# Optimization experiments

Hardware: AMD Instinct MI355X
Metric: run time of the kernel (lower is better)

The kernel has to match this reference:

```python
import jax, jax.numpy as jnp
import numpy as np

B, S, H = 2, 2048, 2048
DK = DV = 128
HK, HV = 16, 32
G = HV // HK          # num_v_groups = 2
K = 4                 # conv kernel size
EPS = 1e-6
FQKVZ = 2 * HK * DK + 2 * HV * DV   # 12288
FBA = 2 * HV                        # 64
C = 2 * HK * DK + HV * DV           # conv channels = 8192


def setup_inputs() -> dict:
    key = jax.random.key(0)
    ks = jax.random.split(key, 10)
    f32 = jnp.float32
    return {
        "x": jax.random.normal(ks[0], (B, S, H), f32),
        "w_qkvz": jax.random.normal(ks[1], (H, FQKVZ), f32) * 0.02,
        "w_ba": jax.random.normal(ks[2], (H, FBA), f32) * 0.02,
        "conv_w": jax.random.normal(ks[3], (C, K), f32) * 0.1,
        "conv_b": jax.random.normal(ks[4], (C,), f32) * 0.02,
        "a_log": jax.random.normal(ks[5], (HV,), f32) * 0.5,
        "dt_bias": jax.random.normal(ks[6], (HV,), f32) * 0.5,
        "norm_w": jnp.ones((DV,), f32),
        "w_o": jax.random.normal(ks[7], (HV * DV, H), f32) * 0.02,
    }


def _l2norm(t):
    return t * jax.lax.rsqrt(jnp.sum(t * t, axis=-1, keepdims=True) + EPS)


def reference(x, w_qkvz, w_ba, conv_w, conv_b, a_log, dt_bias, norm_w, w_o):
    # fused input projections
    qkvz = x @ w_qkvz                                   # [B,S,FQKVZ]
    ba = x @ w_ba                                       # [B,S,FBA]

    # split_fused_inputs: per k-head layout [q(DK), k(DK), v(G*DV), z(G*DV)]
    qkvz = qkvz.reshape(B, S, HK, 2 * DK + 2 * G * DV)
    q = qkvz[..., :DK]                                  # [B,S,HK,DK]
    k = qkvz[..., DK:2 * DK]
    v = qkvz[..., 2 * DK:2 * DK + G * DV].reshape(B, S, HV, DV)
    z = qkvz[..., 2 * DK + G * DV:].reshape(B, S, HV, DV)
    ba = ba.reshape(B, S, HK, 2 * G)
    b = ba[..., :G].reshape(B, S, HV)
    a = ba[..., G:].reshape(B, S, HV)

    # causal depthwise conv1d + silu over concat(q,k,v) channels
    mixed = jnp.concatenate(
        [q.reshape(B, S, HK * DK), k.reshape(B, S, HK * DK), v.reshape(B, S, HV * DV)],
        axis=-1).transpose(0, 2, 1)                     # [B,C,S]
    mixed = jnp.pad(mixed, ((0, 0), (0, 0), (K - 1, 0)))
    mixed = jax.lax.conv_general_dilated(
        mixed, conv_w[:, None, :], (1,), 'VALID',
        dimension_numbers=('NCH', 'OIH', 'NCH'), feature_group_count=C)
    mixed = jax.nn.silu(mixed + conv_b[None, :, None]).transpose(0, 2, 1)  # [B,S,C]

    kd = HK * DK
    q = mixed[..., :kd].reshape(B, S, HK, DK)
    k = mixed[..., kd:2 * kd].reshape(B, S, HK, DK)
    v = mixed[..., 2 * kd:].reshape(B, S, HV, DV)

    # gating params
    g = -jnp.exp(a_log) * jax.nn.softplus(a + dt_bias)  # [B,S,HV]
    beta = jax.nn.sigmoid(b)                            # [B,S,HV]

    # GQA expand + qk l2-norm (kernel applies l2norm inside)
    q = jnp.repeat(q, G, axis=2)                        # [B,S,HV,DK]
    k = jnp.repeat(k, G, axis=2)
    q = _l2norm(q) * (DK ** -0.5)
    k = _l2norm(k)

    # gated delta-rule recurrence: S_t = exp(g_t) S_{t-1} + k_t (beta_t (v_t - k_t^T S))
    def step(Sm, inp):
        q_t, k_t, v_t, g_t, b_t = inp                   # [B,HV,*]
        Sm = Sm * jnp.exp(g_t)[..., None, None]
        kS = jnp.einsum('bhk,bhkv->bhv', k_t, Sm)
        dv = b_t[..., None] * (v_t - kS)
        Sm = Sm + k_t[..., None] * dv[:, :, None, :]
        o_t = jnp.einsum('bhk,bhkv->bhv', q_t, Sm)
        return Sm, o_t

    S0 = jnp.zeros((B, HV, DK, DV), q.dtype)
    seq = (jnp.moveaxis(q, 1, 0), jnp.moveaxis(k, 1, 0), jnp.moveaxis(v, 1, 0),
           jnp.moveaxis(g, 1, 0), jnp.moveaxis(beta, 1, 0))
    _, o = jax.lax.scan(step, S0, seq)                  # o: [S,B,HV,DV]
    o = jnp.moveaxis(o, 0, 1)                           # [B,S,HV,DV]

    # gated RMSNorm (Mamba-style: gate before norm)
    y = o * jax.nn.silu(z)
    var = jnp.mean(y * y, axis=-1, keepdims=True)
    y = y * jax.lax.rsqrt(var + EPS) * norm_w

    return y.reshape(B, S, HV * DV) @ w_o               # [B,S,H]
```

## Files before the change

### kernel.cpp

```cpp
#include <hip/hip_runtime.h>

typedef _Float16 f16;
typedef _Float16 f16x2 __attribute__((ext_vector_type(2)));
typedef _Float16 f16x4 __attribute__((ext_vector_type(4)));
typedef _Float16 f16x8 __attribute__((ext_vector_type(8)));
typedef float f32x4 __attribute__((ext_vector_type(4)));

#define QSCALE 0.08838834764831845f

#define RAW_BARRIER() do { \
    asm volatile("s_waitcnt lgkmcnt(0)" ::: "memory"); \
    __builtin_amdgcn_s_barrier(); \
    __builtin_amdgcn_sched_barrier(0); \
} while (0)

__global__ __launch_bounds__(256) void cvt16_kernel(const float* __restrict__ in,
                                                    f16* __restrict__ out, int n4) {
    int i = blockIdx.x * 256 + threadIdx.x;
    if (i >= n4) return;
    f32x4 v = ((const f32x4*)in)[i];
    f16x4 h;
    h[0] = (f16)v[0]; h[1] = (f16)v[1]; h[2] = (f16)v[2]; h[3] = (f16)v[3];
    ((f16x4*)out)[i] = h;
}

__global__ __launch_bounds__(256) void transpose16_kernel(const float* __restrict__ in,
                                                          f16* __restrict__ out, int R, int C) {
    __shared__ f16 tile[64][66];
    int c0 = blockIdx.x * 64, r0 = blockIdx.y * 64;
    int tid = threadIdx.x;
#pragma unroll
    for (int i = 0; i < 16; ++i) {
        int idx = i * 256 + tid;
        int r = idx >> 6, c = idx & 63;
        tile[r][c] = (f16)in[(long)(r0 + r) * C + (c0 + c)];
    }
    __syncthreads();
#pragma unroll
    for (int i = 0; i < 16; ++i) {
        int idx = i * 256 + tid;
        int orow = idx >> 6, oc = idx & 63;
        out[(long)(c0 + orow) * R + (r0 + oc)] = tile[oc][orow];
    }
}

template <int NJ, int F16OUT>
__global__ __launch_bounds__(512, 1) void gemm256_kernel(const f16* __restrict__ A,
                                                         const f16* __restrict__ Bt,
                                                         void* __restrict__ Cout,
                                                         int M, int N, int Kd) {
    constexpr int BN = 64 * NJ;
    constexpr int BNW = 16 * NJ;
    __shared__ f16 sA[2][256 * 64];
    __shared__ f16 sB[2][BN * 64];
    const int tid = threadIdx.x;
    const int lane = tid & 63, wv = tid >> 6;
    const int wm = wv >> 2, wn = wv & 3;
    const int m0 = blockIdx.y * 256, n0 = blockIdx.x * BN;
    const int lrow = lane & 15, lk = lane >> 4;
    const int nK = Kd >> 6;

    f32x4 acc[8][NJ] = {};
    f32x4 ra[4], rb[NJ];

    auto issue = [&](int k0) {
#pragma unroll
        for (int j = 0; j < 4; ++j) {
            int P = (tid + j * 512) * 16;
            int row = P >> 7;
            int koff = (P & 127) >> 1;
            ra[j] = *(const f32x4*)(A + (long)(m0 + row) * Kd + k0 + koff);
        }
#pragma unroll
        for (int j = 0; j < NJ; ++j) {
            int P = (tid + j * 512) * 16;
            int row = P >> 7;
            int koff = (P & 127) >> 1;
            rb[j] = *(const f32x4*)(Bt + (long)(n0 + row) * Kd + k0 + koff);
        }
    };
    auto commit = [&](int buf) {
#pragma unroll
        for (int j = 0; j < 4; ++j) {
            int P = (tid + j * 512) * 16;
            int row = P >> 7;
            int sw = P ^ ((row & 7) << 4);
            *(f32x4*)((char*)&sA[buf][0] + sw) = ra[j];
        }
#pragma unroll
        for (int j = 0; j < NJ; ++j) {
            int P = (tid + j * 512) * 16;
            int row = P >> 7;
            int sw = P ^ ((row & 7) << 4);
            *(f32x4*)((char*)&sB[buf][0] + sw) = rb[j];
        }
    };

    issue(0);
    commit(0);
    if (nK > 1) issue(64);
    RAW_BARRIER();

    int cur = 0;
    for (int t = 0; t < nK; ++t) {
        if (t + 1 < nK) commit(cur ^ 1);
        if (t + 2 < nK) issue((t + 2) * 64);
        const char* bA = (const char*)&sA[cur][0];
        const char* bB = (const char*)&sB[cur][0];
        __builtin_amdgcn_s_setprio(1);
#pragma unroll
        for (int kk = 0; kk < 2; ++kk) {
            f16x8 bf[NJ];
#pragma unroll
            for (int j = 0; j < NJ; ++j) {
                int brow = wn * BNW + j * 16 + lrow;
                int bbyte = brow * 128 + kk * 64 + lk * 16;
                bf[j] = *(const f16x8*)(bB + (bbyte ^ ((brow & 7) << 4)));
            }
#pragma unroll
            for (int i = 0; i < 8; ++i) {
                int arow = wm * 128 + i * 16 + lrow;
                int abyte = arow * 128 + kk * 64 + lk * 16;
                f16x8 af = *(const f16x8*)(bA + (abyte ^ ((arow & 7) << 4)));
#pragma unroll
                for (int j = 0; j < NJ; ++j)
                    acc[i][j] = __builtin_amdgcn_mfma_f32_16x16x32_f16(af, bf[j], acc[i][j], 0, 0, 0);
            }
        }
        __builtin_amdgcn_s_setprio(0);
        RAW_BARRIER();
        cur ^= 1;
    }

#pragma unroll
    for (int i = 0; i < 8; ++i) {
        int gm_base = m0 + wm * 128 + i * 16 + lk * 4;
#pragma unroll
        for (int j = 0; j < NJ; ++j) {
            int gn = n0 + wn * BNW + j * 16 + lrow;
#pragma unroll
            for (int r = 0; r < 4; ++r) {
                long idx = (long)(gm_base + r) * N + gn;
                if (F16OUT) ((f16*)Cout)[idx] = (f16)acc[i][j][r];
                else        ((float*)Cout)[idx] = acc[i][j][r];
            }
        }
    }
}

__global__ __launch_bounds__(256) void ba_gemm_kernel(const float* __restrict__ x,
                                                      const float* __restrict__ w,
                                                      const float* __restrict__ a_log,
                                                      const float* __restrict__ dt_bias,
                                                      float* __restrict__ gout,
                                                      float* __restrict__ bt) {
    __shared__ float xs[16][256];
    int tid = threadIdx.x;
    int t0 = blockIdx.x * 16;
    int o = tid & 63, tg = tid >> 6;
    float acc[4] = {0.f, 0.f, 0.f, 0.f};
    for (int kc = 0; kc < 2048; kc += 256) {
        __syncthreads();
#pragma unroll
        for (int i = 0; i < 16; ++i) {
            int idx = i * 256 + tid;
            int tok = idx >> 8, k = idx & 255;
            xs[tok][k] = x[(long)(t0 + tok) * 2048 + kc + k];
        }
        __syncthreads();
        for (int k = 0; k < 256; ++k) {
            float wv = w[(long)(kc + k) * 64 + o];
#pragma unroll
            for (int j = 0; j < 4; ++j) acc[j] += xs[tg * 4 + j][k] * wv;
        }
    }
    int hv = ((o >> 2) << 1) | (o & 1);
    bool isB = (o & 2) == 0;
    float al = expf(a_log[hv]);
    float db = dt_bias[hv];
#pragma unroll
    for (int j = 0; j < 4; ++j) {
        int tok = t0 + tg * 4 + j;
        int b = tok >> 11, s = tok & 2047;
        long oidx = ((long)b * 32 + hv) * 2048 + s;
        if (isB) {
            bt[oidx] = 1.f / (1.f + expf(-acc[j]));
        } else {
            float xx = acc[j] + db;
            float sp = (xx > 20.f) ? xx : log1pf(expf(xx));
            gout[oidx] = -al * sp;
        }
    }
}

__global__ __launch_bounds__(256) void conv_kernel(const f16* __restrict__ qkvz,
                                                   const float* __restrict__ cw,
                                                   const float* __restrict__ cb,
                                                   f16* __restrict__ qh,
                                                   f16* __restrict__ kh,
                                                   f16* __restrict__ vh) {
    __shared__ float Lin[35 * 128];
    __shared__ float Lout[32 * 128];
    __shared__ float Lsc[32];
    int g = blockIdx.x;
    int s0 = blockIdx.y * 32;
    int b = blockIdx.z;
    int tid = threadIdx.x;
    int colbase, chbase;
    f16* outp;
    bool donorm;
    float nmul;
    if (g < 16) {
        colbase = g * 768; chbase = g * 128;
        outp = qh + (((long)b * 16 + g) * 2048 + s0) * 128;
        donorm = true; nmul = QSCALE;
    } else if (g < 32) {
        int hk = g - 16;
        colbase = hk * 768 + 128; chbase = 2048 + hk * 128;
        outp = kh + (((long)b * 16 + hk) * 2048 + s0) * 128;
        donorm = true; nmul = 1.f;
    } else {
        int hv = g - 32;
        colbase = (hv >> 1) * 768 + 256 + (hv & 1) * 128; chbase = 4096 + hv * 128;
        outp = vh + (((long)b * 32 + hv) * 2048 + s0) * 128;
        donorm = false; nmul = 1.f;
    }
    for (int ci = tid; ci < 35 * 16; ci += 256) {
        int sr = ci >> 4, cc = (ci & 15) * 8;
        int s = s0 + sr - 3;
        f32x4 lo = {}, hi = {};
        if (s >= 0) {
            f16x8 v = *(const f16x8*)(qkvz + ((long)b * 2048 + s) * 12288 + colbase + cc);
#pragma unroll
            for (int e = 0; e < 4; ++e) { lo[e] = (float)v[e]; hi[e] = (float)v[4 + e]; }
        }
        *(f32x4*)&Lin[sr * 128 + cc] = lo;
        *(f32x4*)&Lin[sr * 128 + cc + 4] = hi;
    }
    __syncthreads();
    int c = tid & 127, sg = tid >> 7;
    float w0 = cw[(chbase + c) * 4 + 0];
    float w1 = cw[(chbase + c) * 4 + 1];
    float w2 = cw[(chbase + c) * 4 + 2];
    float w3 = cw[(chbase + c) * 4 + 3];
    float bias = cb[chbase + c];
#pragma unroll
    for (int j = 0; j < 16; ++j) {
        int sl = sg * 16 + j;
        float v = w0 * Lin[sl * 128 + c] + w1 * Lin[(sl + 1) * 128 + c] +
                  w2 * Lin[(sl + 2) * 128 + c] + w3 * Lin[(sl + 3) * 128 + c] + bias;
        v = v / (1.f + expf(-v));
        Lout[sl * 128 + c] = v;
    }
    __syncthreads();
    if (donorm) {
        int token = tid >> 3, part = tid & 7;
        float ss = 0.f;
#pragma unroll
        for (int i = 0; i < 16; ++i) {
            float v = Lout[token * 128 + part * 16 + i];
            ss += v * v;
        }
        ss += __shfl_xor(ss, 1); ss += __shfl_xor(ss, 2); ss += __shfl_xor(ss, 4);
        if (part == 0) Lsc[token] = rsqrtf(ss + 1e-6f) * nmul;
        __syncthreads();
#pragma unroll
        for (int j = 0; j < 16; ++j) {
            int sl = sg * 16 + j;
            outp[(long)sl * 128 + c] = (f16)(Lout[sl * 128 + c] * Lsc[sl]);
        }
    } else {
#pragma unroll
        for (int j = 0; j < 16; ++j) {
            int sl = sg * 16 + j;
            outp[(long)sl * 128 + c] = (f16)Lout[sl * 128 + c];
        }
    }
}

__global__ __launch_bounds__(256) void kT_kernel(const f16* __restrict__ kh,
                                                 f16* __restrict__ khT) {
    __shared__ f16 t[64][136];
    int bh = blockIdx.x >> 5;
    int s0 = (blockIdx.x & 31) * 64;
    int tid = threadIdx.x;
#pragma unroll
    for (int it = 0; it < 4; ++it) {
        int P = (tid + it * 256) * 8;
        int r = P >> 7, col = P & 127;
        *(f16x8*)&t[r][col] = *(const f16x8*)(kh + ((long)bh * 2048 + s0 + r) * 128 + col);
    }
    __syncthreads();
#pragma unroll
    for (int it = 0; it < 4; ++it) {
        int Q = (tid + it * 256) * 8;
        int dk = Q >> 6, sc = Q & 63;
        f16x8 v;
#pragma unroll
        for (int e = 0; e < 8; ++e) v[e] = t[sc + e][dk];
        *(f16x8*)(khT + ((long)bh * 128 + dk) * 2048 + s0 + sc) = v;
    }
}

__global__ __launch_bounds__(64) void chunk_pre_kernel(const f16* __restrict__ qh,
                                                       const f16* __restrict__ kh,
                                                       const f16* __restrict__ vh,
                                                       const float* __restrict__ gb,
                                                       const float* __restrict__ bt,
                                                       f16* __restrict__ Wg,
                                                       f16* __restrict__ T2ng,
                                                       f16* __restrict__ d0g,
                                                       float* __restrict__ pvg) {
    __shared__ f16 VTl[128 * 32];
    __shared__ float KKl[32 * 32];
    __shared__ float RL[32 * 32];
    __shared__ float Tf[32 * 33];
    __shared__ f16 Tl[32 * 64];
    __shared__ float cuml[32], bl[32], pl[32];

    int bid = blockIdx.x;
    int chunk = bid & 63;
    int hv = (bid >> 6) & 31;
    int b = bid >> 11;
    int bh = b * 16 + (hv >> 1);
    int l = threadIdx.x;
    int h = l >> 4, c = l & 15;
    long chid = bid;

    const f16* kbase = kh + ((long)bh * 2048 + chunk * 32) * 128;
    const f16* qbase = qh + ((long)bh * 2048 + chunk * 32) * 128;
    const f16* vbase = vh + (((long)b * 32 + hv) * 2048 + chunk * 32) * 128;
    const float* gp = gb + ((long)b * 32 + hv) * 2048 + chunk * 32;
    const float* bp = bt + ((long)b * 32 + hv) * 2048 + chunk * 32;

    f16x8 fk[2][4], fq[2][4];
#pragma unroll
    for (int ti = 0; ti < 2; ++ti)
#pragma unroll
        for (int kk = 0; kk < 4; ++kk) {
            fk[ti][kk] = *(const f16x8*)(kbase + (c + 16 * ti) * 128 + kk * 32 + h * 8);
            fq[ti][kk] = *(const f16x8*)(qbase + (c + 16 * ti) * 128 + kk * 32 + h * 8);
        }

    float gv = (l < 32) ? gp[l] : 0.f;
#pragma unroll
    for (int d = 1; d < 32; d <<= 1) {
        float t2 = __shfl_up(gv, d);
        if (l >= d) gv += t2;
    }
    if (l < 32) { cuml[l] = gv; bl[l] = bp[l]; pl[l] = expf(gv); }
    __syncthreads();

#pragma unroll
    for (int it = 0; it < 8; ++it) {
        int idx = (l + it * 64) * 8;
        int row = idx >> 7, col = idx & 127;
        f16x8 v = *(const f16x8*)(vbase + (long)row * 128 + col);
        float be = bl[row];
#pragma unroll
        for (int e = 0; e < 8; ++e) {
            int dv = col + e;
            int byte = (dv * 64 + row * 2) ^ ((dv & 3) << 4);
            *(f16*)((char*)VTl + byte) = (f16)((float)v[e] * be);
        }
    }
#pragma unroll
    for (int it = 0; it < 16; ++it) {
        int e = l * 16 + it;
        int i = e >> 5, j = e & 31;
        RL[e] = (j <= i) ? expf(cuml[i] - cuml[j]) : 0.f;
    }
    __syncthreads();

    {
        f32x4 acc[2][2] = {};
#pragma unroll
        for (int kk = 0; kk < 4; ++kk) {
            acc[0][0] = __builtin_amdgcn_mfma_f32_16x16x32_f16(fk[0][kk], fk[0][kk], acc[0][0], 0, 0, 0);
            acc[0][1] = __builtin_amdgcn_mfma_f32_16x16x32_f16(fk[0][kk], fk[1][kk], acc[0][1], 0, 0, 0);
            acc[1][0] = __builtin_amdgcn_mfma_f32_16x16x32_f16(fk[1][kk], fk[0][kk], acc[1][0], 0, 0, 0);
            acc[1][1] = __builtin_amdgcn_mfma_f32_16x16x32_f16(fk[1][kk], fk[1][kk], acc[1][1], 0, 0, 0);
        }
#pragma unroll
        for (int ti = 0; ti < 2; ++ti)
#pragma unroll
            for (int tj = 0; tj < 2; ++tj)
#pragma unroll
                for (int r = 0; r < 4; ++r)
                    KKl[(h * 4 + r + 16 * ti) * 32 + c + 16 * tj] = acc[ti][tj][r];
    }
    {
        f32x4 acc[2][2] = {};
#pragma unroll
        for (int kk = 0; kk < 4; ++kk) {
            acc[0][0] = __builtin_amdgcn_mfma_f32_16x16x32_f16(fq[0][kk], fk[0][kk], acc[0][0], 0, 0, 0);
            acc[0][1] = __builtin_amdgcn_mfma_f32_16x16x32_f16(fq[0][kk], fk[1][kk], acc[0][1], 0, 0, 0);
            acc[1][0] = __builtin_amdgcn_mfma_f32_16x16x32_f16(fq[1][kk], fk[0][kk], acc[1][0], 0, 0, 0);
            acc[1][1] = __builtin_amdgcn_mfma_f32_16x16x32_f16(fq[1][kk], fk[1][kk], acc[1][1], 0, 0, 0);
        }
        __syncthreads();
#pragma unroll
        for (int ti = 0; ti < 2; ++ti)
#pragma unroll
            for (int tj = 0; tj < 2; ++tj)
#pragma unroll
                for (int r = 0; r < 4; ++r) {
                    int i = h * 4 + r + 16 * ti, j = c + 16 * tj;
                    Wg[chid * 1024 + i * 32 + j] = (f16)(acc[ti][tj][r] * RL[i * 32 + j]);
                }
    }

    if (l < 32) {
        int j = l;
        for (int i = 0; i < 32; ++i) {
            float s = (i == j) ? 1.f : 0.f;
            float bi = bl[i];
            for (int ll = j; ll < i; ++ll)
                s -= bi * KKl[i * 32 + ll] * RL[i * 32 + ll] * Tf[ll * 33 + j];
            Tf[i * 33 + j] = s;
        }
        float bpj = bl[j] * pl[j];
        for (int i = 0; i < 32; ++i) {
            float tv = (i >= j) ? Tf[i * 33 + j] : 0.f;
            int byte = (i * 128 + j * 2) ^ ((i & 3) << 4);
            *(f16*)((char*)Tl + byte) = (f16)tv;
            T2ng[chid * 1024 + i * 32 + j] = (f16)(-tv * bpj);
        }
        pvg[chid * 64 + j] = pl[j];
        pvg[chid * 64 + 32 + j] = expf(cuml[31] - cuml[j]);
    }
    __syncthreads();

    {
        f16x8 fT[2];
#pragma unroll
        for (int ti = 0; ti < 2; ++ti) {
            int row = c + 16 * ti;
            fT[ti] = *(const f16x8*)((const char*)Tl + ((row * 128 + h * 16) ^ ((row & 3) << 4)));
        }
#pragma unroll
        for (int nj = 0; nj < 8; ++nj) {
            int dv = c + 16 * nj;
            f16x8 fv = *(const f16x8*)((const char*)VTl + ((dv * 64 + h * 16) ^ ((dv & 3) << 4)));
            f32x4 a0 = {}, a1 = {};
            a0 = __builtin_amdgcn_mfma_f32_16x16x32_f16(fT[0], fv, a0, 0, 0, 0);
            a1 = __builtin_amdgcn_mfma_f32_16x16x32_f16(fT[1], fv, a1, 0, 0, 0);
            f16x4 s0, s1;
#pragma unroll
            for (int r = 0; r < 4; ++r) { s0[r] = (f16)a0[r]; s1[r] = (f16)a1[r]; }
            *(f16x4*)(d0g + chid * 4096 + (long)dv * 32 + 4 * h) = s0;
            *(f16x4*)(d0g + chid * 4096 + (long)dv * 32 + 16 + 4 * h) = s1;
        }
    }
}

__global__ __launch_bounds__(64) void scan_kernel(const f16* __restrict__ qh,
                                                  const f16* __restrict__ kh,
                                                  const f16* __restrict__ khT,
                                                  const f16* __restrict__ Wg,
                                                  const f16* __restrict__ T2ng,
                                                  const f16* __restrict__ d0g,
                                                  const float* __restrict__ pvg,
                                                  f16* __restrict__ ob) {
    __shared__ f16 Sl[2][16 * 128];
    __shared__ f16 AKl[16 * 32];
    __shared__ f16 Dl[16 * 32];

    int pbid = blockIdx.x;
    int bid = (pbid & 7) * 64 + (pbid >> 3);
    int vs = bid & 7;
    int hv = (bid >> 3) & 31;
    int b = bid >> 8;
    int bh32 = b * 32 + hv;
    int bh = b * 16 + (hv >> 1);
    int l = threadIdx.x, h = l >> 4, c = l & 15;

    const f16* kb = kh + (long)bh * 2048 * 128;
    const f16* qb = qh + (long)bh * 2048 * 128;
    const f16* ktb = khT + (long)bh * 128 * 2048;

    f16x8 z = {};
#pragma unroll
    for (int it = 0; it < 4; ++it) *(f16x8*)((char*)Sl[0] + (l + it * 64) * 16) = z;
    __syncthreads();

    int cur = 0;
    for (int ch = 0; ch < 64; ++ch) {
        long chid = (long)bh32 * 64 + ch;
        f16x8 fk[2][4], fq[2][4], fkt[8], fT[2], fW[2];
#pragma unroll
        for (int ti = 0; ti < 2; ++ti) {
            long row = ch * 32 + c + 16 * ti;
#pragma unroll
            for (int kk = 0; kk < 4; ++kk) {
                fk[ti][kk] = *(const f16x8*)(kb + row * 128 + kk * 32 + h * 8);
                fq[ti][kk] = *(const f16x8*)(qb + row * 128 + kk * 32 + h * 8);
            }
            fT[ti] = *(const f16x8*)(T2ng + chid * 1024 + (c + 16 * ti) * 32 + h * 8);
            fW[ti] = *(const f16x8*)(Wg + chid * 1024 + (c + 16 * ti) * 32 + h * 8);
        }
#pragma unroll
        for (int ti = 0; ti < 8; ++ti)
            fkt[ti] = *(const f16x8*)(ktb + (long)(c + 16 * ti) * 2048 + ch * 32 + h * 8);
        f16x4 fd0[2];
#pragma unroll
        for (int ti = 0; ti < 2; ++ti)
            fd0[ti] = *(const f16x4*)(d0g + chid * 4096 +
                                      (long)(vs * 16 + c) * 32 + 16 * ti + 4 * h);
        f32x4 pva = *(const f32x4*)(pvg + chid * 64 + 4 * h);
        f32x4 pvb = *(const f32x4*)(pvg + chid * 64 + 16 + 4 * h);
        float pc = pvg[chid * 64 + 31];
        f32x4 kwa = *(const f32x4*)(pvg + chid * 64 + 32 + h * 8);
        f32x4 kwb = *(const f32x4*)(pvg + chid * 64 + 36 + h * 8);

        const int dv = c;
        f16x8 fS[4];
#pragma unroll
        for (int kk = 0; kk < 4; ++kk)
            fS[kk] = *(const f16x8*)((char*)Sl[cur] +
                                     (dv * 256 + ((kk * 64 + h * 16) ^ ((dv & 7) << 4))));
        f32x4 AK[2] = {}, AQ[2] = {};
#pragma unroll
        for (int ti = 0; ti < 2; ++ti)
#pragma unroll
            for (int kk = 0; kk < 4; ++kk) {
                AK[ti] = __builtin_amdgcn_mfma_f32_16x16x32_f16(fk[ti][kk], fS[kk], AK[ti], 0, 0, 0);
                AQ[ti] = __builtin_amdgcn_mfma_f32_16x16x32_f16(fq[ti][kk], fS[kk], AQ[ti], 0, 0, 0);
            }
#pragma unroll
        for (int ti = 0; ti < 2; ++ti) {
            f16x4 t;
#pragma unroll
            for (int r = 0; r < 4; ++r) t[r] = (f16)AK[ti][r];
            *(f16x4*)((char*)AKl + ((dv * 64 + 32 * ti + 8 * h) ^ ((dv & 3) << 4))) = t;
        }
        f32x4 Dv[2];
#pragma unroll
        for (int ti = 0; ti < 2; ++ti)
#pragma unroll
            for (int r = 0; r < 4; ++r) Dv[ti][r] = (float)fd0[ti][r];
        {
            f16x8 fak = *(const f16x8*)((char*)AKl + ((dv * 64 + h * 16) ^ ((dv & 3) << 4)));
#pragma unroll
            for (int ti = 0; ti < 2; ++ti)
                Dv[ti] = __builtin_amdgcn_mfma_f32_16x16x32_f16(fT[ti], fak, Dv[ti], 0, 0, 0);
        }
#pragma unroll
        for (int ti = 0; ti < 2; ++ti) {
            f16x4 t;
#pragma unroll
            for (int r = 0; r < 4; ++r) t[r] = (f16)Dv[ti][r];
            *(f16x4*)((char*)Dl + ((dv * 64 + 32 * ti + 8 * h) ^ ((dv & 3) << 4))) = t;
        }
        f16x8 fdl = *(const f16x8*)((char*)Dl + ((dv * 64 + h * 16) ^ ((dv & 3) << 4)));
        f32x4 Ov[2];
#pragma unroll
        for (int ti = 0; ti < 2; ++ti)
#pragma unroll
            for (int r = 0; r < 4; ++r)
                Ov[ti][r] = AQ[ti][r] * (ti ? pvb[r] : pva[r]);
#pragma unroll
        for (int ti = 0; ti < 2; ++ti)
            Ov[ti] = __builtin_amdgcn_mfma_f32_16x16x32_f16(fW[ti], fdl, Ov[ti], 0, 0, 0);
#pragma unroll
        for (int ti = 0; ti < 2; ++ti)
#pragma unroll
            for (int r = 0; r < 4; ++r) {
                long tok = (long)b * 2048 + ch * 32 + 16 * ti + 4 * h + r;
                ob[tok * 4096 + hv * 128 + vs * 16 + c] = (f16)Ov[ti][r];
            }
#pragma unroll
        for (int ti = 0; ti < 8; ++ti) {
            f16x8 fa;
#pragma unroll
            for (int e = 0; e < 8; ++e)
                fa[e] = (f16)((float)fkt[ti][e] * (e < 4 ? kwa[e] : kwb[e - 4]));
            int sbyte = (dv * 256 + (32 * ti + 8 * h)) ^ ((dv & 7) << 4);
            f16x4 sold = *(const f16x4*)((char*)Sl[cur] + sbyte);
            f32x4 acc;
#pragma unroll
            for (int r = 0; r < 4; ++r) acc[r] = pc * (float)sold[r];
            acc = __builtin_amdgcn_mfma_f32_16x16x32_f16(fa, fdl, acc, 0, 0, 0);
            f16x4 snew;
#pragma unroll
            for (int r = 0; r < 4; ++r) snew[r] = (f16)acc[r];
            *(f16x4*)((char*)Sl[cur ^ 1] + sbyte) = snew;
        }
        cur ^= 1;
        __syncthreads();
    }
}

__global__ __launch_bounds__(256) void gate_kernel(const f16* __restrict__ o,
                                                   const f16* __restrict__ qkvz,
                                                   const float* __restrict__ norm_w,
                                                   f16* __restrict__ y) {
    int token = blockIdx.x;
    int tid = threadIdx.x;
    int hv = tid >> 3, part = tid & 7;
    int dv0 = part * 16;
    const f16* orow = o + ((long)token * 32 + hv) * 128 + dv0;
    long zcol = (long)(hv >> 1) * 768 + 512 + (hv & 1) * 128 + dv0;
    const f16* zrow = qkvz + (long)token * 12288 + zcol;
    f16x8 ov0 = *(const f16x8*)orow, ov1 = *(const f16x8*)(orow + 8);
    f16x8 zv0 = *(const f16x8*)zrow, zv1 = *(const f16x8*)(zrow + 8);
    float yv[16];
    float ss = 0.f;
#pragma unroll
    for (int i = 0; i < 16; ++i) {
        float ovf = (float)(i < 8 ? ov0[i] : ov1[i - 8]);
        float zvf = (float)(i < 8 ? zv0[i] : zv1[i - 8]);
        float gt = zvf / (1.f + expf(-zvf));
        float v = ovf * gt;
        yv[i] = v;
        ss += v * v;
    }
    ss += __shfl_xor(ss, 1); ss += __shfl_xor(ss, 2); ss += __shfl_xor(ss, 4);
    float scale = rsqrtf(ss * (1.f / 128.f) + 1e-6f);
    f16* yrow = y + (long)token * 4096 + hv * 128 + dv0;
    f16x8 y0, y1;
#pragma unroll
    for (int i = 0; i < 8; ++i) {
        y0[i] = (f16)(yv[i] * scale * norm_w[dv0 + i]);
        y1[i] = (f16)(yv[8 + i] * scale * norm_w[dv0 + 8 + i]);
    }
    *(f16x8*)yrow = y0;
    *(f16x8*)(yrow + 8) = y1;
}

extern "C" void kernel_launch(void* const* d_in, const int* in_sizes, int n_in,
                              void* d_out, int out_size, void* d_ws, size_t ws_size,
                              hipStream_t stream) {
    const float* x       = (const float*)d_in[0];
    const float* w_qkvz  = (const float*)d_in[1];
    const float* w_ba    = (const float*)d_in[2];
    const float* conv_w  = (const float*)d_in[3];
    const float* conv_b  = (const float*)d_in[4];
    const float* a_log   = (const float*)d_in[5];
    const float* dt_bias = (const float*)d_in[6];
    const float* norm_w  = (const float*)d_in[7];
    const float* w_o     = (const float*)d_in[8];
    float* out = (float*)d_out;

    char* ws = (char*)d_ws;
    const size_t MB = 1024 * 1024;
    f16*   qkvz16 = (f16*)ws;
    f16*   x16    = (f16*)(ws + 96 * MB);
    f16*   WT     = (f16*)(ws + 112 * MB);
    f16*   d0g    = (f16*)(ws + 96 * MB);
    f16*   Wg     = (f16*)(ws + 128 * MB);
    f16*   T2ng   = (f16*)(ws + 136 * MB);
    f16*   khT    = (f16*)(ws + 144 * MB);
    f16*   WTo    = (f16*)(ws + 160 * MB);
    f16*   qh     = (f16*)(ws + 176 * MB);
    f16*   kh     = (f16*)(ws + 192 * MB);
    f16*   vh     = (f16*)(ws + 208 * MB);
    f16*   ob     = (f16*)(ws + 208 * MB);
    f16*   y16    = (f16*)(ws + 176 * MB);
    float* gbuf   = (float*)(ws + 240 * MB);
    float* btb    = (float*)(ws + 240 * MB + 512 * 1024);
    float* pvg    = (float*)(ws + 241 * MB);

    cvt16_kernel<<<8192, 256, 0, stream>>>(x, x16, 4096 * 2048 / 4);
    transpose16_kernel<<<dim3(12288 / 64, 2048 / 64), 256, 0, stream>>>(w_qkvz, WT, 2048, 12288);
    transpose16_kernel<<<dim3(2048 / 64, 4096 / 64), 256, 0, stream>>>(w_o, WTo, 4096, 2048);

    gemm256_kernel<4, 1><<<dim3(12288 / 256, 4096 / 256), 512, 0, stream>>>(x16, WT, qkvz16, 4096, 12288, 2048);
    ba_gemm_kernel<<<256, 256, 0, stream>>>(x, w_ba, a_log, dt_bias, gbuf, btb);

    conv_kernel<<<dim3(64, 64, 2), 256, 0, stream>>>(qkvz16, conv_w, conv_b, qh, kh, vh);
    kT_kernel<<<1024, 256, 0, stream>>>(kh, khT);
    chunk_pre_kernel<<<4096, 64, 0, stream>>>(qh, kh, vh, gbuf, btb, Wg, T2ng, d0g, pvg);
    scan_kernel<<<512, 64, 0, stream>>>(qh, kh, khT, Wg, T2ng, d0g, pvg, ob);

    gate_kernel<<<4096, 256, 0, stream>>>(ob, qkvz16, norm_w, y16);

    gemm256_kernel<2, 0><<<dim3(2048 / 128, 4096 / 256), 512, 0, stream>>>(y16, WTo, out, 4096, 2048, 4096);
}
```

Measured before the change: 820.9 us.

## Fuse k transpose into conv and software-pipeline scan chunk loads

The conv kernel now also writes the transposed, normalized k (khT) straight from shared memory, which removes the separate kT_kernel launch and its extra read/write pass over k. The scan kernel is restructured so the global loads for the next chunk are issued into a second register set while the current chunk computes (double-buffered registers), and it uses raw barriers with launch_bounds(64,1). This should hide global load latency on the serial chunk recurrence. The cost is higher register pressure, and the khT writes in conv are strided 16-byte stores.

```diff
diff --git a/kernel.cpp b/kernel.cpp
--- a/kernel.cpp
+++ b/kernel.cpp
@@ -198,7 +198,8 @@
                                                    const float* __restrict__ cb,
                                                    f16* __restrict__ qh,
                                                    f16* __restrict__ kh,
-                                                   f16* __restrict__ vh) {
+                                                   f16* __restrict__ vh,
+                                                   f16* __restrict__ khT) {
     __shared__ float Lin[35 * 128];
     __shared__ float Lout[32 * 128];
     __shared__ float Lsc[32];
@@ -209,16 +210,18 @@
     int colbase, chbase;
     f16* outp;
     bool donorm;
+    bool isk = false;
+    int hk = 0;
     float nmul;
     if (g < 16) {
         colbase = g * 768; chbase = g * 128;
         outp = qh + (((long)b * 16 + g) * 2048 + s0) * 128;
         donorm = true; nmul = QSCALE;
     } else if (g < 32) {
-        int hk = g - 16;
+        hk = g - 16;
         colbase = hk * 768 + 128; chbase = 2048 + hk * 128;
         outp = kh + (((long)b * 16 + hk) * 2048 + s0) * 128;
-        donorm = true; nmul = 1.f;
+        donorm = true; nmul = 1.f; isk = true;
     } else {
         int hv = g - 32;
         colbase = (hv >> 1) * 768 + 256 + (hv & 1) * 128; chbase = 4096 + hv * 128;
@@ -269,36 +272,24 @@
             int sl = sg * 16 + j;
             outp[(long)sl * 128 + c] = (f16)(Lout[sl * 128 + c] * Lsc[sl]);
         }
+        if (isk) {
+            int dk = tid >> 1, sh = tid & 1;
+            f16x8 v0, v1;
+#pragma unroll
+            for (int i = 0; i < 8; ++i) {
+                v0[i] = (f16)(Lout[(sh * 16 + i) * 128 + dk] * Lsc[sh * 16 + i]);
+                v1[i] = (f16)(Lout[(sh * 16 + 8 + i) * 128 + dk] * Lsc[sh * 16 + 8 + i]);
+            }
+            f16* kt = khT + ((long)(b * 16 + hk) * 128 + dk) * 2048 + s0 + sh * 16;
+            *(f16x8*)kt = v0;
+            *(f16x8*)(kt + 8) = v1;
+        }
     } else {
 #pragma unroll
         for (int j = 0; j < 16; ++j) {
             int sl = sg * 16 + j;
             outp[(long)sl * 128 + c] = (f16)Lout[sl * 128 + c];
         }
-    }
-}
-
-__global__ __launch_bounds__(256) void kT_kernel(const f16* __restrict__ kh,
-                                                 f16* __restrict__ khT) {
-    __shared__ f16 t[64][136];
-    int bh = blockIdx.x >> 5;
-    int s0 = (blockIdx.x & 31) * 64;
-    int tid = threadIdx.x;
-#pragma unroll
-    for (int it = 0; it < 4; ++it) {
-        int P = (tid + it * 256) * 8;
-        int r = P >> 7, col = P & 127;
-        *(f16x8*)&t[r][col] = *(const f16x8*)(kh + ((long)bh * 2048 + s0 + r) * 128 + col);
-    }
-    __syncthreads();
-#pragma unroll
-    for (int it = 0; it < 4; ++it) {
-        int Q = (tid + it * 256) * 8;
-        int dk = Q >> 6, sc = Q & 63;
-        f16x8 v;
-#pragma unroll
-        for (int e = 0; e < 8; ++e) v[e] = t[sc + e][dk];
-        *(f16x8*)(khT + ((long)bh * 128 + dk) * 2048 + s0 + sc) = v;
     }
 }
 
@@ -454,14 +445,21 @@
     }
 }
 
-__global__ __launch_bounds__(64) void scan_kernel(const f16* __restrict__ qh,
-                                                  const f16* __restrict__ kh,
-                                                  const f16* __restrict__ khT,
-                                                  const f16* __restrict__ Wg,
-                                                  const f16* __restrict__ T2ng,
-                                                  const f16* __restrict__ d0g,
-                                                  const float* __restrict__ pvg,
-                                                  f16* __restrict__ ob) {
+struct CR {
+    f16x8 fk[2][4], fq[2][4], fkt[8], fT[2], fW[2];
+    f16x4 fd0[2];
+    f32x4 pva, pvb, kwa, kwb;
+    float pc;
+};
+
+__global__ __launch_bounds__(64, 1) void scan_kernel(const f16* __restrict__ qh,
+                                                     const f16* __restrict__ kh,
+                                                     const f16* __restrict__ khT,
+                                                     const f16* __restrict__ Wg,
+                                                     const f16* __restrict__ T2ng,
+                                                     const f16* __restrict__ d0g,
+                                                     const float* __restrict__ pvg,
+                                                     f16* __restrict__ ob) {
     __shared__ f16 Sl[2][16 * 128];
     __shared__ f16 AKl[16 * 32];
     __shared__ f16 Dl[16 * 32];
@@ -482,37 +480,37 @@
     f16x8 z = {};
 #pragma unroll
     for (int it = 0; it < 4; ++it) *(f16x8*)((char*)Sl[0] + (l + it * 64) * 16) = z;
-    __syncthreads();
 
     int cur = 0;
-    for (int ch = 0; ch < 64; ++ch) {
+
+    auto loadC = [&](CR& R, int ch) {
         long chid = (long)bh32 * 64 + ch;
-        f16x8 fk[2][4], fq[2][4], fkt[8], fT[2], fW[2];
 #pragma unroll
         for (int ti = 0; ti < 2; ++ti) {
-            long row = ch * 32 + c + 16 * ti;
+            long row = (long)ch * 32 + c + 16 * ti;
 #pragma unroll
             for (int kk = 0; kk < 4; ++kk) {
-                fk[ti][kk] = *(const f16x8*)(kb + row * 128 + kk * 32 + h * 8);
-                fq[ti][kk] = *(const f16x8*)(qb + row * 128 + kk * 32 + h * 8);
+                R.fk[ti][kk] = *(const f16x8*)(kb + row * 128 + kk * 32 + h * 8);
+                R.fq[ti][kk] = *(const f16x8*)(qb + row * 128 + kk * 32 + h * 8);
             }
-            fT[ti] = *(const f16x8*)(T2ng + chid * 1024 + (c + 16 * ti) * 32 + h * 8);
-            fW[ti] = *(const f16x8*)(Wg + chid * 1024 + (c + 16 * ti) * 32 + h * 8);
+            R.fT[ti] = *(const f16x8*)(T2ng + chid * 1024 + (c + 16 * ti) * 32 + h * 8);
+            R.fW[ti] = *(const f16x8*)(Wg + chid * 1024 + (c + 16 * ti) * 32 + h * 8);
         }
 #pragma unroll
         for (int ti = 0; ti < 8; ++ti)
-            fkt[ti] = *(const f16x8*)(ktb + (long)(c + 16 * ti) * 2048 + ch * 32 + h * 8);
-        f16x4 fd0[2];
-#pragma unroll
-        for (int ti = 0; ti < 2; ++ti)
-            fd0[ti] = *(const f16x4*)(d0g + chid * 4096 +
-                                      (long)(vs * 16 + c) * 32 + 16 * ti + 4 * h);
-        f32x4 pva = *(const f32x4*)(pvg + chid * 64 + 4 * h);
-        f32x4 pvb = *(const f32x4*)(pvg + chid * 64 + 16 + 4 * h);
-        float pc = pvg[chid * 64 + 31];
-        f32x4 kwa = *(const f32x4*)(pvg + chid * 64 + 32 + h * 8);
-        f32x4 kwb = *(const f32x4*)(pvg + chid * 64 + 36 + h * 8);
-
+            R.fkt[ti] = *(const f16x8*)(ktb + (long)(c + 16 * ti) * 2048 + ch * 32 + h * 8);
+#pragma unroll
+        for (int ti = 0; ti < 2; ++ti)
+            R.fd0[ti] = *(const f16x4*)(d0g + chid * 4096 +
+                                        (long)(vs * 16 + c) * 32 + 16 * ti + 4 * h);
+        R.pva = *(const f32x4*)(pvg + chid * 64 + 4 * h);
+        R.pvb = *(const f32x4*)(pvg + chid * 64 + 16 + 4 * h);
+        R.pc = pvg[chid * 64 + 31];
+        R.kwa = *(const f32x4*)(pvg + chid * 64 + 32 + h * 8);
+        R.kwb = *(const f32x4*)(pvg + chid * 64 + 36 + h * 8);
+    };
+
+    auto computeC = [&](const CR& R, int ch) {
         const int dv = c;
         f16x8 fS[4];
 #pragma unroll
@@ -524,8 +522,8 @@
         for (int ti = 0; ti < 2; ++ti)
 #pragma unroll
             for (int kk = 0; kk < 4; ++kk) {
-                AK[ti] = __builtin_amdgcn_mfma_f32_16x16x32_f16(fk[ti][kk], fS[kk], AK[ti], 0, 0, 0);
-                AQ[ti] = __builtin_amdgcn_mfma_f32_16x16x32_f16(fq[ti][kk], fS[kk], AQ[ti], 0, 0, 0);
+                AK[ti] = __builtin_amdgcn_mfma_f32_16x16x32_f16(R.fk[ti][kk], fS[kk], AK[ti], 0, 0, 0);
+                AQ[ti] = __builtin_amdgcn_mfma_f32_16x16x32_f16(R.fq[ti][kk], fS[kk], AQ[ti], 0, 0, 0);
             }
 #pragma unroll
         for (int ti = 0; ti < 2; ++ti) {
@@ -538,12 +536,12 @@
 #pragma unroll
         for (int ti = 0; ti < 2; ++ti)
 #pragma unroll
-            for (int r = 0; r < 4; ++r) Dv[ti][r] = (float)fd0[ti][r];
+            for (int r = 0; r < 4; ++r) Dv[ti][r] = (float)R.fd0[ti][r];
         {
             f16x8 fak = *(const f16x8*)((char*)AKl + ((dv * 64 + h * 16) ^ ((dv & 3) << 4)));
 #pragma unroll
             for (int ti = 0; ti < 2; ++ti)
-                Dv[ti] = __builtin_amdgcn_mfma_f32_16x16x32_f16(fT[ti], fak, Dv[ti], 0, 0, 0);
+                Dv[ti] = __builtin_amdgcn_mfma_f32_16x16x32_f16(R.fT[ti], fak, Dv[ti], 0, 0, 0);
         }
 #pragma unroll
         for (int ti = 0; ti < 2; ++ti) {
@@ -558,10 +556,10 @@
         for (int ti = 0; ti < 2; ++ti)
 #pragma unroll
             for (int r = 0; r < 4; ++r)
-                Ov[ti][r] = AQ[ti][r] * (ti ? pvb[r] : pva[r]);
-#pragma unroll
-        for (int ti = 0; ti < 2; ++ti)
-            Ov[ti] = __builtin_amdgcn_mfma_f32_16x16x32_f16(fW[ti], fdl, Ov[ti], 0, 0, 0);
+                Ov[ti][r] = AQ[ti][r] * (ti ? R.pvb[r] : R.pva[r]);
+#pragma unroll
+        for (int ti = 0; ti < 2; ++ti)
+            Ov[ti] = __builtin_amdgcn_mfma_f32_16x16x32_f16(R.fW[ti], fdl, Ov[ti], 0, 0, 0);
 #pragma unroll
         for (int ti = 0; ti < 2; ++ti)
 #pragma unroll
@@ -574,12 +572,12 @@
             f16x8 fa;
 #pragma unroll
             for (int e = 0; e < 8; ++e)
-                fa[e] = (f16)((float)fkt[ti][e] * (e < 4 ? kwa[e] : kwb[e - 4]));
+                fa[e] = (f16)((float)R.fkt[ti][e] * (e < 4 ? R.kwa[e] : R.kwb[e - 4]));
             int sbyte = (dv * 256 + (32 * ti + 8 * h)) ^ ((dv & 7) << 4);
             f16x4 sold = *(const f16x4*)((char*)Sl[cur] + sbyte);
             f32x4 acc;
 #pragma unroll
-            for (int r = 0; r < 4; ++r) acc[r] = pc * (float)sold[r];
+            for (int r = 0; r < 4; ++r) acc[r] = R.pc * (float)sold[r];
             acc = __builtin_amdgcn_mfma_f32_16x16x32_f16(fa, fdl, acc, 0, 0, 0);
             f16x4 snew;
 #pragma unroll
@@ -587,7 +585,17 @@
             *(f16x4*)((char*)Sl[cur ^ 1] + sbyte) = snew;
         }
         cur ^= 1;
-        __syncthreads();
+        RAW_BARRIER();
+    };
+
+    CR A, B;
+    loadC(A, 0);
+    RAW_BARRIER();
+    for (int ch = 0; ch < 64; ch += 2) {
+        loadC(B, ch + 1);
+        computeC(A, ch);
+        loadC(A, ch + 2 < 64 ? ch + 2 : 63);
+        computeC(B, ch + 1);
     }
 }
 
@@ -668,8 +676,7 @@
     gemm256_kernel<4, 1><<<dim3(12288 / 256, 4096 / 256), 512, 0, stream>>>(x16, WT, qkvz16, 4096, 12288, 2048);
     ba_gemm_kernel<<<256, 256, 0, stream>>>(x, w_ba, a_log, dt_bias, gbuf, btb);
 
-    conv_kernel<<<dim3(64, 64, 2), 256, 0, stream>>>(qkvz16, conv_w, conv_b, qh, kh, vh);
-    kT_kernel<<<1024, 256, 0, stream>>>(kh, khT);
+    conv_kernel<<<dim3(64, 64, 2), 256, 0, stream>>>(qkvz16, conv_w, conv_b, qh, kh, vh, khT);
     chunk_pre_kernel<<<4096, 64, 0, stream>>>(qh, kh, vh, gbuf, btb, Wg, T2ng, d0g, pvg);
     scan_kernel<<<512, 64, 0, stream>>>(qh, kh, khT, Wg, T2ng, d0g, pvg, ob);
 
```

Result: faster. 748.0 us (-8.9%).
